# Kernel tuning notes

Hardware: AMD Instinct MI355X
Metric: run time of the kernel (lower is better)

The kernel has to match this reference:

```python
import jax, jax.numpy as jnp
import numpy as np

B, S, D = 4, 4096, 256

def setup_inputs() -> dict:
    key = jax.random.key(0)
    k1, k2 = jax.random.split(key)
    x = jax.random.normal(k1, (B, S, D), dtype=jnp.float32)
    # xavier_uniform for Linear(D, 2D): bound = sqrt(6/(fan_in+fan_out))
    bound = np.sqrt(6.0 / (D + 2 * D))
    W = jax.random.uniform(k2, (2 * D, D), dtype=jnp.float32, minval=-bound, maxval=bound)
    b = jnp.zeros((2 * D,), dtype=jnp.float32)
    return {"x": x, "W": W, "b": b}

def reference(x, W, b):
    # qk projection: [B,S,2D]
    qk = jnp.einsum('bsd,ed->bse', x, W) + b
    q, k = jnp.split(qk, 2, axis=-1)            # each [B,S,D]
    v = x
    scale = 1.0 / np.sqrt(D)
    logits = jnp.einsum('bqd,bkd->bqk', q, k) * scale   # [B,S,S]
    attn = jax.nn.softmax(logits, axis=-1)
    values = jnp.einsum('bqk,bkd->bqd', attn, v)        # [B,S,D]
    return values.sum(axis=1)                           # [B,D] sum-pool over queries
```

## Files before the change

### kernel.cpp

```cpp
#include <hip/hip_runtime.h>
#include <stdint.h>

typedef __bf16 v8bf __attribute__((ext_vector_type(8)));
typedef float  v4f  __attribute__((ext_vector_type(4)));
typedef int    v4i  __attribute__((ext_vector_type(4)));
typedef unsigned short u16;
typedef unsigned char  u8;

static constexpr int B_ = 4, S_ = 4096, D_ = 256, E_ = 512;
static constexpr float QSC_ = 127.0f / 4.8f;
static constexpr float DQ_  = 1.288045e-4f;

#define AS1C(p) ((const __attribute__((address_space(1))) void*)(p))
#define AS3(p)  ((__attribute__((address_space(3))) void*)(p))

__device__ __forceinline__ v8bf ldfrag(const u16* p) {
    return __builtin_bit_cast(v8bf, *(const uint4*)p);
}
__device__ __forceinline__ u16 f2bf(float f) {
    return __builtin_bit_cast(u16, (__bf16)f);
}
__device__ __forceinline__ u8 f2i8(float f) {
    float t = fminf(fmaxf(f * QSC_, -127.f), 127.f);
    return (u8)(signed char)__float2int_rn(t);
}

__global__ void k_convw(const float* __restrict__ Wf, u16* __restrict__ Wb,
                        float* __restrict__ Z, float* __restrict__ w,
                        float* __restrict__ out) {
    int i = blockIdx.x * 256 + threadIdx.x;
    Wb[i] = f2bf(Wf[i]);
    if (i < B_ * S_) { Z[i] = 0.f; w[i] = 0.f; }
    if (i < B_ * D_) out[i] = 0.f;
}

__global__ __launch_bounds__(256) void k_proj(const float* __restrict__ x,
                                              const u16* __restrict__ Wb,
                                              const float* __restrict__ bias,
                                              u8* __restrict__ Qi,
                                              u8* __restrict__ Ki) {
    const int tid = threadIdx.x, wave = tid >> 6, lane = tid & 63;
    const int l15 = lane & 15, quad = lane >> 4;
    const int tt = blockIdx.x * 2 + (wave >> 1);
    const int wsel = wave & 1;
    const int tbase = tt * 16;

    v8bf a[8];
    const float* xrow = x + (size_t)(tbase + l15) * D_ + quad * 8;
#pragma unroll
    for (int j = 0; j < 8; ++j) {
        float4 f0 = *(const float4*)(xrow + j * 32);
        float4 f1 = *(const float4*)(xrow + j * 32 + 4);
        v8bf t;
        t[0] = (__bf16)f0.x; t[1] = (__bf16)f0.y; t[2] = (__bf16)f0.z; t[3] = (__bf16)f0.w;
        t[4] = (__bf16)f1.x; t[5] = (__bf16)f1.y; t[6] = (__bf16)f1.z; t[7] = (__bf16)f1.w;
        a[j] = t;
    }

    u8* dst = wsel ? Ki : Qi;
    const u16* wbase = Wb + (size_t)(wsel * 256 + l15) * D_ + quad * 8;
    const float* bb = bias + wsel * 256;

    v8bf wcur[8], wnxt[8];
#pragma unroll
    for (int j = 0; j < 8; ++j) wcur[j] = ldfrag(wbase + j * 32);

    auto tile = [&](const v8bf (&wb)[8], int nt) {
        v4f acc = {0.f, 0.f, 0.f, 0.f};
#pragma unroll
        for (int j = 0; j < 8; ++j)
            acc = __builtin_amdgcn_mfma_f32_16x16x32_bf16(a[j], wb[j], acc, 0, 0, 0);
        const int col = nt * 16 + l15;
        const float bv = bb[col];
#pragma unroll
        for (int r = 0; r < 4; ++r) {
            const int tok = tbase + quad * 4 + r;
            dst[tok * D_ + col] = f2i8(acc[r] + bv);
        }
    };

    for (int nt = 0; nt < 16; nt += 2) {
        const u16* wp1 = wbase + (size_t)(nt + 1) * 16 * D_;
#pragma unroll
        for (int j = 0; j < 8; ++j) wnxt[j] = ldfrag(wp1 + j * 32);
        tile(wcur, nt);
        if (nt + 2 < 16) {
            const u16* wp2 = wbase + (size_t)(nt + 2) * 16 * D_;
#pragma unroll
            for (int j = 0; j < 8; ++j) wcur[j] = ldfrag(wp2 + j * 32);
        }
        tile(wnxt, nt + 1);
    }
}

__device__ __forceinline__ void stage64(const u8* src, u8* dst,
                                        int wave, int lane) {
#pragma unroll
    for (int v = 0; v < 4; ++v) {
        const int sbase = v * 256 + wave * 64;
        const int slot = sbase + lane;
        const int R = slot >> 4, P = slot & 15;
        const int c = P ^ (R & 15);
        __builtin_amdgcn_global_load_lds(AS1C(src + R * 256 + c * 16),
                                         AS3(dst + sbase * 16), 16, 0, 0);
    }
}

__global__ __launch_bounds__(256, 2) void k_passA(const u8* __restrict__ Qi,
                                                  const u8* __restrict__ Ki,
                                                  float* __restrict__ Z) {
    __shared__ u8 sK[2][16384];
    const int tid = threadIdx.x, wave = tid >> 6, lane = tid & 63;
    const int l15 = lane & 15, quad = lane >> 4;
    const int blk = blockIdx.x;
    const int ks = blk & 7;
    const int qg = (blk >> 3) & 15;
    const int b = blk >> 7;
    const int qbase = qg * 256 + wave * 64;
    const int kstart = ks * 512;

    v4i a[4][4];
    {
        const u8* qp = Qi + (size_t)(b * S_ + qbase + l15) * D_ + quad * 16;
#pragma unroll
        for (int s = 0; s < 4; ++s)
#pragma unroll
            for (int c = 0; c < 4; ++c)
                a[s][c] = *(const v4i*)(qp + s * 16 * D_ + c * 64);
    }
    float z[4][4];
#pragma unroll
    for (int s = 0; s < 4; ++s)
#pragma unroll
        for (int r = 0; r < 4; ++r) z[s][r] = 0.f;

    const u8* kb = Ki + (size_t)(b * S_ + kstart) * D_;
    stage64(kb, sK[0], wave, lane);

    for (int t = 0; t < 8; ++t) {
        __syncthreads();
        if (t + 1 < 8) stage64(kb + (size_t)(t + 1) * 64 * D_, sK[(t + 1) & 1], wave, lane);
        const u8* base = sK[t & 1];
#pragma unroll
        for (int u = 0; u < 4; ++u) {
            v4i bf[4];
#pragma unroll
            for (int kc = 0; kc < 4; ++kc) {
                const int P = (kc * 4 + quad) ^ l15;
                bf[kc] = *(const v4i*)(base + (u * 16 + l15) * 256 + P * 16);
            }
            v4i c0 = {0,0,0,0}, c1 = {0,0,0,0}, c2 = {0,0,0,0}, c3 = {0,0,0,0};
#pragma unroll
            for (int kc = 0; kc < 4; ++kc) {
                c0 = __builtin_amdgcn_mfma_i32_16x16x64_i8(a[0][kc], bf[kc], c0, 0, 0, 0);
                c1 = __builtin_amdgcn_mfma_i32_16x16x64_i8(a[1][kc], bf[kc], c1, 0, 0, 0);
                c2 = __builtin_amdgcn_mfma_i32_16x16x64_i8(a[2][kc], bf[kc], c2, 0, 0, 0);
                c3 = __builtin_amdgcn_mfma_i32_16x16x64_i8(a[3][kc], bf[kc], c3, 0, 0, 0);
            }
#pragma unroll
            for (int r = 0; r < 4; ++r) {
                z[0][r] += __builtin_amdgcn_exp2f((float)c0[r] * DQ_);
                z[1][r] += __builtin_amdgcn_exp2f((float)c1[r] * DQ_);
                z[2][r] += __builtin_amdgcn_exp2f((float)c2[r] * DQ_);
                z[3][r] += __builtin_amdgcn_exp2f((float)c3[r] * DQ_);
            }
        }
    }

#pragma unroll
    for (int s = 0; s < 4; ++s)
#pragma unroll
        for (int r = 0; r < 4; ++r) {
            float v = z[s][r];
#pragma unroll
            for (int off = 1; off < 16; off <<= 1) v += __shfl_xor(v, off);
            if (l15 == 0) atomicAdd(&Z[b * S_ + qbase + s * 16 + quad * 4 + r], v);
        }
}

__global__ __launch_bounds__(256, 2) void k_passB(const u8* __restrict__ Qi,
                                                  const u8* __restrict__ Ki,
                                                  const float* __restrict__ Zs,
                                                  float* __restrict__ w) {
    __shared__ u8 sQ[2][16384];
    const int tid = threadIdx.x, wave = tid >> 6, lane = tid & 63;
    const int l15 = lane & 15, quad = lane >> 4;
    const int blk = blockIdx.x;
    const int qs = blk & 7;
    const int kg = (blk >> 3) & 15;
    const int b = blk >> 7;
    const int kbase = kg * 256 + wave * 64;
    const int qstart = qs * 512;

    v4i bk[4][4];
    {
        const u8* kp = Ki + (size_t)(b * S_ + kbase + l15) * D_ + quad * 16;
#pragma unroll
        for (int s = 0; s < 4; ++s)
#pragma unroll
            for (int c = 0; c < 4; ++c)
                bk[s][c] = *(const v4i*)(kp + s * 16 * D_ + c * 64);
    }
    float wsum[4] = {0.f, 0.f, 0.f, 0.f};

    const u8* qb = Qi + (size_t)(b * S_ + qstart) * D_;
    stage64(qb, sQ[0], wave, lane);
    const float* zrow = Zs + b * S_ + qstart + quad * 4;

    for (int t = 0; t < 8; ++t) {
        __syncthreads();
        if (t + 1 < 8) stage64(qb + (size_t)(t + 1) * 64 * D_, sQ[(t + 1) & 1], wave, lane);
        const u8* base = sQ[t & 1];
#pragma unroll
        for (int u = 0; u < 4; ++u) {
            const float4 Zv = *(const float4*)(zrow + t * 64 + u * 16);
            v4i af[4];
#pragma unroll
            for (int kc = 0; kc < 4; ++kc) {
                const int P = (kc * 4 + quad) ^ l15;
                af[kc] = *(const v4i*)(base + (u * 16 + l15) * 256 + P * 16);
            }
            v4i c0 = {0,0,0,0}, c1 = {0,0,0,0}, c2 = {0,0,0,0}, c3 = {0,0,0,0};
#pragma unroll
            for (int kc = 0; kc < 4; ++kc) {
                c0 = __builtin_amdgcn_mfma_i32_16x16x64_i8(af[kc], bk[0][kc], c0, 0, 0, 0);
                c1 = __builtin_amdgcn_mfma_i32_16x16x64_i8(af[kc], bk[1][kc], c1, 0, 0, 0);
                c2 = __builtin_amdgcn_mfma_i32_16x16x64_i8(af[kc], bk[2][kc], c2, 0, 0, 0);
                c3 = __builtin_amdgcn_mfma_i32_16x16x64_i8(af[kc], bk[3][kc], c3, 0, 0, 0);
            }
            const float rz0 = __builtin_amdgcn_rcpf(Zv.x);
            const float rz1 = __builtin_amdgcn_rcpf(Zv.y);
            const float rz2 = __builtin_amdgcn_rcpf(Zv.z);
            const float rz3 = __builtin_amdgcn_rcpf(Zv.w);
            wsum[0] += __builtin_amdgcn_exp2f((float)c0[0] * DQ_) * rz0 + __builtin_amdgcn_exp2f((float)c0[1] * DQ_) * rz1
                     + __builtin_amdgcn_exp2f((float)c0[2] * DQ_) * rz2 + __builtin_amdgcn_exp2f((float)c0[3] * DQ_) * rz3;
            wsum[1] += __builtin_amdgcn_exp2f((float)c1[0] * DQ_) * rz0 + __builtin_amdgcn_exp2f((float)c1[1] * DQ_) * rz1
                     + __builtin_amdgcn_exp2f((float)c1[2] * DQ_) * rz2 + __builtin_amdgcn_exp2f((float)c1[3] * DQ_) * rz3;
            wsum[2] += __builtin_amdgcn_exp2f((float)c2[0] * DQ_) * rz0 + __builtin_amdgcn_exp2f((float)c2[1] * DQ_) * rz1
                     + __builtin_amdgcn_exp2f((float)c2[2] * DQ_) * rz2 + __builtin_amdgcn_exp2f((float)c2[3] * DQ_) * rz3;
            wsum[3] += __builtin_amdgcn_exp2f((float)c3[0] * DQ_) * rz0 + __builtin_amdgcn_exp2f((float)c3[1] * DQ_) * rz1
                     + __builtin_amdgcn_exp2f((float)c3[2] * DQ_) * rz2 + __builtin_amdgcn_exp2f((float)c3[3] * DQ_) * rz3;
        }
    }

#pragma unroll
    for (int s = 0; s < 4; ++s) {
        wsum[s] += __shfl_xor(wsum[s], 16);
        wsum[s] += __shfl_xor(wsum[s], 32);
        if (quad == 0) atomicAdd(&w[b * S_ + kbase + s * 16 + l15], wsum[s]);
    }
}

__global__ __launch_bounds__(256) void k_final(const float* __restrict__ x,
                                               const float* __restrict__ w,
                                               float* __restrict__ out) {
    const int b = blockIdx.x >> 7, kc = blockIdx.x & 127;
    const int d = threadIdx.x;
    const int k0 = kc * 32;
    float acc = 0.f;
    const float* xp = x + (size_t)(b * S_ + k0) * D_ + d;
    const float* wp = w + b * S_ + k0;
#pragma unroll 8
    for (int kk = 0; kk < 32; ++kk) acc += wp[kk] * xp[(size_t)kk * D_];
    atomicAdd(&out[b * D_ + d], acc);
}

extern "C" void kernel_launch(void* const* d_in, const int* in_sizes, int n_in,
                              void* d_out, int out_size, void* d_ws, size_t ws_size,
                              hipStream_t stream) {
    const float* x    = (const float*)d_in[0];
    const float* W    = (const float*)d_in[1];
    const float* bias = (const float*)d_in[2];
    float* out = (float*)d_out;

    char* ws = (char*)d_ws;
    u8*    Qi = (u8*)ws;
    u8*    Ki = Qi + (size_t)B_ * S_ * D_;
    float* Z  = (float*)(ws + 8388608);
    float* w  = Z + B_ * S_;
    u16*   Wb = (u16*)(w + B_ * S_);

    k_convw<<<E_ * D_ / 256, 256, 0, stream>>>(W, Wb, Z, w, out);
    k_proj <<<512, 256, 0, stream>>>(x, Wb, bias, Qi, Ki);
    k_passA<<<512, 256, 0, stream>>>(Qi, Ki, Z);
    k_passB<<<512, 256, 0, stream>>>(Qi, Ki, Z, w);
    k_final<<<512, 256, 0, stream>>>(x, w, out);
}
```

Baseline: 155.5 us.

## Drop weight-conversion kernel, replace atomics with per-split partial buffers

Removes the separate W-to-bf16 conversion and zero-init kernel: k_proj now converts fp32 weights on the fly, and only the output is cleared with a memset. Pass A and pass B write per-split partial sums into slices instead of using atomicAdd. Pass B reduces the eight Z partials into a shared reciprocal table, and k_final sums the eight w partials. This saves one launch and the atomic traffic, at the cost of redundant weight loads and conversions in k_proj, extra partial reads, and fewer final blocks.

```diff
diff --git a/kernel.cpp b/kernel.cpp
--- a/kernel.cpp
+++ b/kernel.cpp
@@ -14,28 +14,21 @@
 #define AS1C(p) ((const __attribute__((address_space(1))) void*)(p))
 #define AS3(p)  ((__attribute__((address_space(3))) void*)(p))
 
-__device__ __forceinline__ v8bf ldfrag(const u16* p) {
-    return __builtin_bit_cast(v8bf, *(const uint4*)p);
-}
-__device__ __forceinline__ u16 f2bf(float f) {
-    return __builtin_bit_cast(u16, (__bf16)f);
-}
 __device__ __forceinline__ u8 f2i8(float f) {
     float t = fminf(fmaxf(f * QSC_, -127.f), 127.f);
     return (u8)(signed char)__float2int_rn(t);
 }
-
-__global__ void k_convw(const float* __restrict__ Wf, u16* __restrict__ Wb,
-                        float* __restrict__ Z, float* __restrict__ w,
-                        float* __restrict__ out) {
-    int i = blockIdx.x * 256 + threadIdx.x;
-    Wb[i] = f2bf(Wf[i]);
-    if (i < B_ * S_) { Z[i] = 0.f; w[i] = 0.f; }
-    if (i < B_ * D_) out[i] = 0.f;
+__device__ __forceinline__ v8bf cvt8(const float* p) {
+    float4 f0 = *(const float4*)p;
+    float4 f1 = *(const float4*)(p + 4);
+    v8bf t;
+    t[0] = (__bf16)f0.x; t[1] = (__bf16)f0.y; t[2] = (__bf16)f0.z; t[3] = (__bf16)f0.w;
+    t[4] = (__bf16)f1.x; t[5] = (__bf16)f1.y; t[6] = (__bf16)f1.z; t[7] = (__bf16)f1.w;
+    return t;
 }
 
 __global__ __launch_bounds__(256) void k_proj(const float* __restrict__ x,
-                                              const u16* __restrict__ Wb,
+                                              const float* __restrict__ W,
                                               const float* __restrict__ bias,
                                               u8* __restrict__ Qi,
                                               u8* __restrict__ Ki) {
@@ -48,22 +41,15 @@
     v8bf a[8];
     const float* xrow = x + (size_t)(tbase + l15) * D_ + quad * 8;
 #pragma unroll
-    for (int j = 0; j < 8; ++j) {
-        float4 f0 = *(const float4*)(xrow + j * 32);
-        float4 f1 = *(const float4*)(xrow + j * 32 + 4);
-        v8bf t;
-        t[0] = (__bf16)f0.x; t[1] = (__bf16)f0.y; t[2] = (__bf16)f0.z; t[3] = (__bf16)f0.w;
-        t[4] = (__bf16)f1.x; t[5] = (__bf16)f1.y; t[6] = (__bf16)f1.z; t[7] = (__bf16)f1.w;
-        a[j] = t;
-    }
+    for (int j = 0; j < 8; ++j) a[j] = cvt8(xrow + j * 32);
 
     u8* dst = wsel ? Ki : Qi;
-    const u16* wbase = Wb + (size_t)(wsel * 256 + l15) * D_ + quad * 8;
+    const float* wbase = W + (size_t)(wsel * 256 + l15) * D_ + quad * 8;
     const float* bb = bias + wsel * 256;
 
     v8bf wcur[8], wnxt[8];
 #pragma unroll
-    for (int j = 0; j < 8; ++j) wcur[j] = ldfrag(wbase + j * 32);
+    for (int j = 0; j < 8; ++j) wcur[j] = cvt8(wbase + j * 32);
 
     auto tile = [&](const v8bf (&wb)[8], int nt) {
         v4f acc = {0.f, 0.f, 0.f, 0.f};
@@ -80,14 +66,14 @@
     };
 
     for (int nt = 0; nt < 16; nt += 2) {
-        const u16* wp1 = wbase + (size_t)(nt + 1) * 16 * D_;
-#pragma unroll
-        for (int j = 0; j < 8; ++j) wnxt[j] = ldfrag(wp1 + j * 32);
+        const float* wp1 = wbase + (size_t)(nt + 1) * 16 * D_;
+#pragma unroll
+        for (int j = 0; j < 8; ++j) wnxt[j] = cvt8(wp1 + j * 32);
         tile(wcur, nt);
         if (nt + 2 < 16) {
-            const u16* wp2 = wbase + (size_t)(nt + 2) * 16 * D_;
-#pragma unroll
-            for (int j = 0; j < 8; ++j) wcur[j] = ldfrag(wp2 + j * 32);
+            const float* wp2 = wbase + (size_t)(nt + 2) * 16 * D_;
+#pragma unroll
+            for (int j = 0; j < 8; ++j) wcur[j] = cvt8(wp2 + j * 32);
         }
         tile(wnxt, nt + 1);
     }
@@ -108,7 +94,7 @@
 
 __global__ __launch_bounds__(256, 2) void k_passA(const u8* __restrict__ Qi,
                                                   const u8* __restrict__ Ki,
-                                                  float* __restrict__ Z) {
+                                                  float* __restrict__ Zp) {
     __shared__ u8 sK[2][16384];
     const int tid = threadIdx.x, wave = tid >> 6, lane = tid & 63;
     const int l15 = lane & 15, quad = lane >> 4;
@@ -167,6 +153,7 @@
         }
     }
 
+    float* zdst = Zp + (size_t)ks * B_ * S_ + b * S_ + qbase;
 #pragma unroll
     for (int s = 0; s < 4; ++s)
 #pragma unroll
@@ -174,15 +161,16 @@
             float v = z[s][r];
 #pragma unroll
             for (int off = 1; off < 16; off <<= 1) v += __shfl_xor(v, off);
-            if (l15 == 0) atomicAdd(&Z[b * S_ + qbase + s * 16 + quad * 4 + r], v);
+            if (l15 == 0) zdst[s * 16 + quad * 4 + r] = v;
         }
 }
 
 __global__ __launch_bounds__(256, 2) void k_passB(const u8* __restrict__ Qi,
                                                   const u8* __restrict__ Ki,
-                                                  const float* __restrict__ Zs,
-                                                  float* __restrict__ w) {
+                                                  const float* __restrict__ Zp,
+                                                  float* __restrict__ wp) {
     __shared__ u8 sQ[2][16384];
+    __shared__ float sRZ[512];
     const int tid = threadIdx.x, wave = tid >> 6, lane = tid & 63;
     const int l15 = lane & 15, quad = lane >> 4;
     const int blk = blockIdx.x;
@@ -205,7 +193,15 @@
 
     const u8* qb = Qi + (size_t)(b * S_ + qstart) * D_;
     stage64(qb, sQ[0], wave, lane);
-    const float* zrow = Zs + b * S_ + qstart + quad * 4;
+
+#pragma unroll
+    for (int i = tid; i < 512; i += 256) {
+        float zs = 0.f;
+#pragma unroll
+        for (int p = 0; p < 8; ++p)
+            zs += Zp[(size_t)p * B_ * S_ + b * S_ + qstart + i];
+        sRZ[i] = __builtin_amdgcn_rcpf(zs);
+    }
 
     for (int t = 0; t < 8; ++t) {
         __syncthreads();
@@ -213,7 +209,7 @@
         const u8* base = sQ[t & 1];
 #pragma unroll
         for (int u = 0; u < 4; ++u) {
-            const float4 Zv = *(const float4*)(zrow + t * 64 + u * 16);
+            const v4f rzv = *(const v4f*)(&sRZ[t * 64 + u * 16 + quad * 4]);
             v4i af[4];
 #pragma unroll
             for (int kc = 0; kc < 4; ++kc) {
@@ -228,40 +224,42 @@
                 c2 = __builtin_amdgcn_mfma_i32_16x16x64_i8(af[kc], bk[2][kc], c2, 0, 0, 0);
                 c3 = __builtin_amdgcn_mfma_i32_16x16x64_i8(af[kc], bk[3][kc], c3, 0, 0, 0);
             }
-            const float rz0 = __builtin_amdgcn_rcpf(Zv.x);
-            const float rz1 = __builtin_amdgcn_rcpf(Zv.y);
-            const float rz2 = __builtin_amdgcn_rcpf(Zv.z);
-            const float rz3 = __builtin_amdgcn_rcpf(Zv.w);
-            wsum[0] += __builtin_amdgcn_exp2f((float)c0[0] * DQ_) * rz0 + __builtin_amdgcn_exp2f((float)c0[1] * DQ_) * rz1
-                     + __builtin_amdgcn_exp2f((float)c0[2] * DQ_) * rz2 + __builtin_amdgcn_exp2f((float)c0[3] * DQ_) * rz3;
-            wsum[1] += __builtin_amdgcn_exp2f((float)c1[0] * DQ_) * rz0 + __builtin_amdgcn_exp2f((float)c1[1] * DQ_) * rz1
-                     + __builtin_amdgcn_exp2f((float)c1[2] * DQ_) * rz2 + __builtin_amdgcn_exp2f((float)c1[3] * DQ_) * rz3;
-            wsum[2] += __builtin_amdgcn_exp2f((float)c2[0] * DQ_) * rz0 + __builtin_amdgcn_exp2f((float)c2[1] * DQ_) * rz1
-                     + __builtin_amdgcn_exp2f((float)c2[2] * DQ_) * rz2 + __builtin_amdgcn_exp2f((float)c2[3] * DQ_) * rz3;
-            wsum[3] += __builtin_amdgcn_exp2f((float)c3[0] * DQ_) * rz0 + __builtin_amdgcn_exp2f((float)c3[1] * DQ_) * rz1
-                     + __builtin_amdgcn_exp2f((float)c3[2] * DQ_) * rz2 + __builtin_amdgcn_exp2f((float)c3[3] * DQ_) * rz3;
-        }
-    }
-
+            wsum[0] += __builtin_amdgcn_exp2f((float)c0[0] * DQ_) * rzv[0] + __builtin_amdgcn_exp2f((float)c0[1] * DQ_) * rzv[1]
+                     + __builtin_amdgcn_exp2f((float)c0[2] * DQ_) * rzv[2] + __builtin_amdgcn_exp2f((float)c0[3] * DQ_) * rzv[3];
+            wsum[1] += __builtin_amdgcn_exp2f((float)c1[0] * DQ_) * rzv[0] + __builtin_amdgcn_exp2f((float)c1[1] * DQ_) * rzv[1]
+                     + __builtin_amdgcn_exp2f((float)c1[2] * DQ_) * rzv[2] + __builtin_amdgcn_exp2f((float)c1[3] * DQ_) * rzv[3];
+            wsum[2] += __builtin_amdgcn_exp2f((float)c2[0] * DQ_) * rzv[0] + __builtin_amdgcn_exp2f((float)c2[1] * DQ_) * rzv[1]
+                     + __builtin_amdgcn_exp2f((float)c2[2] * DQ_) * rzv[2] + __builtin_amdgcn_exp2f((float)c2[3] * DQ_) * rzv[3];
+            wsum[3] += __builtin_amdgcn_exp2f((float)c3[0] * DQ_) * rzv[0] + __builtin_amdgcn_exp2f((float)c3[1] * DQ_) * rzv[1]
+                     + __builtin_amdgcn_exp2f((float)c3[2] * DQ_) * rzv[2] + __builtin_amdgcn_exp2f((float)c3[3] * DQ_) * rzv[3];
+        }
+    }
+
+    float* wdst = wp + (size_t)qs * B_ * S_ + b * S_ + kbase;
 #pragma unroll
     for (int s = 0; s < 4; ++s) {
         wsum[s] += __shfl_xor(wsum[s], 16);
         wsum[s] += __shfl_xor(wsum[s], 32);
-        if (quad == 0) atomicAdd(&w[b * S_ + kbase + s * 16 + l15], wsum[s]);
+        if (quad == 0) wdst[s * 16 + l15] = wsum[s];
     }
 }
 
 __global__ __launch_bounds__(256) void k_final(const float* __restrict__ x,
-                                               const float* __restrict__ w,
+                                               const float* __restrict__ wp,
                                                float* __restrict__ out) {
-    const int b = blockIdx.x >> 7, kc = blockIdx.x & 127;
+    const int b = blockIdx.x >> 5, kc = blockIdx.x & 31;
     const int d = threadIdx.x;
-    const int k0 = kc * 32;
+    const int k0 = kc * 128;
     float acc = 0.f;
     const float* xp = x + (size_t)(b * S_ + k0) * D_ + d;
-    const float* wp = w + b * S_ + k0;
-#pragma unroll 8
-    for (int kk = 0; kk < 32; ++kk) acc += wp[kk] * xp[(size_t)kk * D_];
+#pragma unroll 4
+    for (int kk = 0; kk < 128; ++kk) {
+        float wk = 0.f;
+#pragma unroll
+        for (int p = 0; p < 8; ++p)
+            wk += wp[(size_t)p * B_ * S_ + b * S_ + k0 + kk];
+        acc += wk * xp[(size_t)kk * D_];
+    }
     atomicAdd(&out[b * D_ + d], acc);
 }
 
@@ -276,13 +274,12 @@
     char* ws = (char*)d_ws;
     u8*    Qi = (u8*)ws;
     u8*    Ki = Qi + (size_t)B_ * S_ * D_;
-    float* Z  = (float*)(ws + 8388608);
-    float* w  = Z + B_ * S_;
-    u16*   Wb = (u16*)(w + B_ * S_);
-
-    k_convw<<<E_ * D_ / 256, 256, 0, stream>>>(W, Wb, Z, w, out);
-    k_proj <<<512, 256, 0, stream>>>(x, Wb, bias, Qi, Ki);
-    k_passA<<<512, 256, 0, stream>>>(Qi, Ki, Z);
-    k_passB<<<512, 256, 0, stream>>>(Qi, Ki, Z, w);
-    k_final<<<512, 256, 0, stream>>>(x, w, out);
-}
+    float* Zp = (float*)(ws + 8388608);
+    float* wp = Zp + 8 * B_ * S_;
+
+    hipMemsetAsync(out, 0, B_ * D_ * sizeof(float), stream);
+    k_proj <<<512, 256, 0, stream>>>(x, W, bias, Qi, Ki);
+    k_passA<<<512, 256, 0, stream>>>(Qi, Ki, Zp);
+    k_passB<<<512, 256, 0, stream>>>(Qi, Ki, Zp, wp);
+    k_final<<<128, 256, 0, stream>>>(x, wp, out);
+}
```

Measured after the change: 191.9 us. 23.5% more time.
